# Performance work log

Measured on AMD Instinct MI355X. Metric: run time of the kernel, lower is better.

## Reference

```python
import jax, jax.numpy as jnp
import numpy as np

N_NODES = 100000
N_EDGES = 1600000
D_IN = 128
D_HID = 128
D_OUT = 16
N_LAYERS = 3
N_GRAPHS = 64
EPS = 1e-12


def _glorot(key, shape):
    fan_in = shape[-1]
    bound = 1.0 / np.sqrt(fan_in)
    return jax.random.uniform(key, shape, jnp.float32, -bound, bound)


def setup_inputs() -> dict:
    key = jax.random.key(0)
    ks = jax.random.split(key, 12)
    x = jax.random.normal(ks[0], (N_NODES, D_IN), jnp.float32)
    edge_index = jax.random.randint(ks[1], (2, N_EDGES), 0, N_NODES, jnp.int64)
    batch = jnp.sort(jax.random.randint(ks[2], (N_NODES,), 0, N_GRAPHS, jnp.int64))
    # stacked GraphSage weights: torch Linear stores [out, in]
    Wl = _glorot(ks[3], (N_LAYERS, D_HID, D_IN))
    bl = _glorot(ks[4], (N_LAYERS, D_HID))
    Wr = _glorot(ks[5], (N_LAYERS, D_HID, D_IN))
    br = _glorot(ks[6], (N_LAYERS, D_HID))
    W1 = _glorot(ks[7], (D_HID, D_HID))
    b1 = _glorot(ks[8], (D_HID,))
    W2 = _glorot(ks[9], (D_OUT, D_HID))
    b2 = _glorot(ks[10], (D_OUT,))
    return {"x": x, "edge_index": edge_index, "batch": batch,
            "Wl": Wl, "bl": bl, "Wr": Wr, "br": br,
            "W1": W1, "b1": b1, "W2": W2, "b2": b2}


def reference(x, edge_index, batch, Wl, bl, Wr, br, W1, b1, W2, b2):
    N = x.shape[0]
    src, dst = edge_index[0], edge_index[1]
    # in-degree for mean aggregation (clamped to avoid div-by-zero)
    deg = jax.ops.segment_sum(jnp.ones_like(dst, dtype=x.dtype), dst, num_segments=N)
    deg = jnp.maximum(deg, 1.0)[:, None]
    h = x
    for i in range(N_LAYERS):
        # lin_r applied at nodes, then gathered (equivalent to lin_r(x_j) per edge)
        hr = h @ Wr[i].T + br[i]
        msg = hr[src]                               # [E, D_HID] gather
        agg = jax.ops.segment_sum(msg, dst, num_segments=N) / deg  # scatter-mean
        out = agg + (h @ Wl[i].T + bl[i])
        # F.normalize(out) -> L2 norm along dim=1, eps=1e-12
        nrm = jnp.maximum(jnp.linalg.norm(out, axis=1, keepdims=True), EPS)
        h = jax.nn.relu(out / nrm)                  # dropout is identity (eval)
    # post message-passing MLP (dropout identity in eval mode)
    h = h @ W1.T + b1
    h = h @ W2.T + b2
    # global mean pool over graphs
    cnt = jnp.maximum(jax.ops.segment_sum(jnp.ones_like(batch, dtype=h.dtype), batch, num_segments=N_GRAPHS), 1.0)
    pooled = jax.ops.segment_sum(h, batch, num_segments=N_GRAPHS) / cnt[:, None]
    return jax.nn.log_softmax(pooled, axis=1)
```

## Files before the change

### kernel.cpp

```cpp
#include <hip/hip_runtime.h>
#include <cstdint>
#include <cstddef>

#define NN 100000
#define NE 1600000
#define DD 128
#define NG 64
#define NB 782
#define GB 1563

#if defined(__has_builtin)
#if __has_builtin(__builtin_amdgcn_cvt_pk_f32_fp8) && __has_builtin(__builtin_amdgcn_cvt_pk_fp8_f32)
#define USE_FP8 1
#endif
#endif
#ifndef USE_FP8
#define USE_FP8 0
#endif

using bf16x8 = __attribute__((ext_vector_type(8))) short;
using f32x4  = __attribute__((ext_vector_type(4))) float;
using f32x2  = __attribute__((ext_vector_type(2))) float;

__device__ __forceinline__ int clampi(int v, int hi) {
    v = v < 0 ? 0 : v;
    return v >= hi ? hi - 1 : v;
}
__device__ __forceinline__ unsigned short f2bf(float f) {
    unsigned int u = __float_as_uint(f);
    u += 0x7fffu + ((u >> 16) & 1u);
    return (unsigned short)(u >> 16);
}
__device__ __forceinline__ float bf2f(unsigned short s) {
    return __uint_as_float(((unsigned int)s) << 16);
}
#if USE_FP8
__device__ __forceinline__ unsigned char f2fp8(float v) {
    return (unsigned char)(__builtin_amdgcn_cvt_pk_fp8_f32(v, 0.f, 0, false) & 0xFF);
}
#endif

#define WTOT (3 * 256 * 128)
__global__ void cvtw_kernel(const float* __restrict__ Wl, const float* __restrict__ Wr,
                            unsigned short* __restrict__ Wcat2,
                            int* __restrict__ bcnt, int* __restrict__ gcur0,
                            float* __restrict__ pooled, float* __restrict__ cnt) {
    int i = blockIdx.x * 256 + threadIdx.x;
    if (i < NB) { bcnt[i] = 0; gcur0[i] = 0; }
    if (i < NG * DD) pooled[i] = 0.f;
    if (i < NG) cnt[i] = 0.f;
    if (i < WTOT) {
        int l = i >> 15;
        int rem = i & 32767;
        int o = rem >> 7, k = rem & 127;
        float v = (o < 128) ? Wl[(size_t)l * 16384 + o * 128 + k]
                            : Wr[(size_t)l * 16384 + (o - 128) * 128 + k];
        Wcat2[i] = f2bf(v);
    }
}

template <bool F32IN>
__global__ __launch_bounds__(256) void gemm3_kernel(
    const void* __restrict__ hin_, const unsigned short* __restrict__ Wcat2,
    const float* __restrict__ bl, unsigned short* __restrict__ zb,
    unsigned char* __restrict__ ub, const int* __restrict__ dst,
    int* __restrict__ bcnt, int nG) {
    __shared__ unsigned short sstz[64][136];
    __shared__ unsigned char  sstu[64][272];

    if (blockIdx.x >= nG) {
        int* lcnt = (int*)&sstz[0][0];
        for (int i = threadIdx.x; i < NB; i += 256) lcnt[i] = 0;
        __syncthreads();
        int b = blockIdx.x - nG;
        int e0 = b * 8000;
        int e1 = e0 + 8000; if (e1 > NE) e1 = NE;
        for (int e = e0 + threadIdx.x; e < e1; e += 256)
            atomicAdd(&lcnt[clampi(dst[e], NN) >> 7], 1);
        __syncthreads();
        for (int i = threadIdx.x; i < NB; i += 256)
            if (lcnt[i]) atomicAdd(&bcnt[i], lcnt[i]);
        return;
    }

    const int tid = threadIdx.x;
    const int w = tid >> 6, l = tid & 63;
    const int l15 = l & 15, lg = l >> 4;
    const int half = w >> 1, rt = w & 1;
    const int rbase = blockIdx.x * 64 + rt * 32;

    bf16x8 a[4][2];
#pragma unroll
    for (int m = 0; m < 2; ++m) {
        int node = rbase + m * 16 + l15; node = node < NN ? node : NN - 1;
        if (F32IN) {
            const float* hf = (const float*)hin_;
#pragma unroll
            for (int ks = 0; ks < 4; ++ks) {
                const float4 f0 = *(const float4*)(hf + (size_t)node * DD + ks * 32 + lg * 8);
                const float4 f1 = *(const float4*)(hf + (size_t)node * DD + ks * 32 + lg * 8 + 4);
                bf16x8 t;
                t[0] = (short)f2bf(f0.x); t[1] = (short)f2bf(f0.y);
                t[2] = (short)f2bf(f0.z); t[3] = (short)f2bf(f0.w);
                t[4] = (short)f2bf(f1.x); t[5] = (short)f2bf(f1.y);
                t[6] = (short)f2bf(f1.z); t[7] = (short)f2bf(f1.w);
                a[ks][m] = t;
            }
        } else {
            const unsigned short* hb = (const unsigned short*)hin_;
#pragma unroll
            for (int ks = 0; ks < 4; ++ks)
                a[ks][m] = *(const bf16x8*)(hb + (size_t)node * DD + ks * 32 + lg * 8);
        }
    }

    f32x4 acc[2][8];
#pragma unroll
    for (int m = 0; m < 2; ++m)
#pragma unroll
        for (int n = 0; n < 8; ++n) acc[m][n] = (f32x4){0.f, 0.f, 0.f, 0.f};

    const unsigned short* Wb = Wcat2 + half * 128 * 128;
#pragma unroll
    for (int ks = 0; ks < 4; ++ks) {
#pragma unroll
        for (int n = 0; n < 8; ++n) {
            bf16x8 b = *(const bf16x8*)(Wb + (n * 16 + l15) * 128 + ks * 32 + lg * 8);
            acc[0][n] = __builtin_amdgcn_mfma_f32_16x16x32_bf16(a[ks][0], b, acc[0][n], 0, 0, 0);
            acc[1][n] = __builtin_amdgcn_mfma_f32_16x16x32_bf16(a[ks][1], b, acc[1][n], 0, 0, 0);
        }
    }

    if (half == 0) {
        float blv[8];
#pragma unroll
        for (int n = 0; n < 8; ++n) blv[n] = bl[n * 16 + l15];
#pragma unroll
        for (int m = 0; m < 2; ++m)
#pragma unroll
            for (int r = 0; r < 4; ++r) {
                int brow = rt * 32 + m * 16 + lg * 4 + r;
#pragma unroll
                for (int n = 0; n < 8; ++n)
                    sstz[brow][n * 16 + l15] = f2bf(acc[m][n][r] + blv[n]);
            }
#pragma unroll
        for (int p = 0; p < 8; ++p) {
            int brow = rt * 32 + p * 4 + lg;
            int node = blockIdx.x * 64 + brow;
            bf16x8 vv = *(const bf16x8*)(&sstz[brow][l15 * 8]);
            if (node < NN)
                *(bf16x8*)(zb + (size_t)node * DD + l15 * 8) = vv;
        }
    } else {
#pragma unroll
        for (int m = 0; m < 2; ++m)
#pragma unroll
            for (int r = 0; r < 4; ++r) {
                int brow = rt * 32 + m * 16 + lg * 4 + r;
#pragma unroll
                for (int n = 0; n < 8; ++n) {
#if USE_FP8
                    sstu[brow][n * 16 + l15] = f2fp8(acc[m][n][r]);
#else
                    ((unsigned short*)&sstu[brow][0])[n * 16 + l15] = f2bf(acc[m][n][r]);
#endif
                }
            }
#pragma unroll
        for (int p = 0; p < 8; ++p) {
            int brow = rt * 32 + p * 4 + lg;
            int node = blockIdx.x * 64 + brow;
#if USE_FP8
            uint2 vv = *(const uint2*)(&sstu[brow][l15 * 8]);
            if (node < NN)
                *(uint2*)(ub + (size_t)node * DD + l15 * 8) = vv;
#else
            bf16x8 vv = *(const bf16x8*)((unsigned short*)&sstu[brow][0] + l15 * 8);
            if (node < NN)
                *(bf16x8*)((unsigned short*)ub + (size_t)node * DD + l15 * 8) = vv;
#endif
        }
    }
}

__global__ __launch_bounds__(256) void bpart2_kernel(
    const int* __restrict__ src, const int* __restrict__ dst,
    const int* __restrict__ bcnt, int* __restrict__ gcur0,
    int* __restrict__ bstart_g, uint2* __restrict__ stage) {
    __shared__ int bst[NB];
    __shared__ int lcnt[NB];
    __shared__ int partial[256];
    const int t = threadIdx.x;
    int own[4]; int ssum = 0;
#pragma unroll
    for (int q = 0; q < 4; ++q) {
        int idx = t * 4 + q;
        own[q] = (idx < NB) ? bcnt[idx] : 0;
        ssum += own[q];
    }
    partial[t] = ssum;
    __syncthreads();
    for (int d = 1; d < 256; d <<= 1) {
        int v = (t >= d) ? partial[t - d] : 0;
        __syncthreads();
        partial[t] += v;
        __syncthreads();
    }
    int run = partial[t] - ssum;
#pragma unroll
    for (int q = 0; q < 4; ++q) {
        int idx = t * 4 + q;
        if (idx < NB) bst[idx] = run;
        run += own[q];
    }
    if (blockIdx.x == 0) {
#pragma unroll
        for (int q = 0; q < 4; ++q) {
            int idx = t * 4 + q;
            if (idx < NB) bstart_g[idx] = bst[idx];
        }
        if (t == 0) bstart_g[NB] = NE;
    }
    for (int i = t; i < NB; i += 256) lcnt[i] = 0;
    __syncthreads();
    int e0 = blockIdx.x * 8000;
    int e1 = e0 + 8000; if (e1 > NE) e1 = NE;
    for (int e = e0 + t; e < e1; e += 256)
        atomicAdd(&lcnt[clampi(dst[e], NN) >> 7], 1);
    __syncthreads();
    for (int i = t; i < NB; i += 256) {
        int c = lcnt[i];
        if (c) lcnt[i] = bst[i] + atomicAdd(&gcur0[i], c);
    }
    __syncthreads();
    for (int e = e0 + t; e < e1; e += 256) {
        int d = clampi(dst[e], NN);
        int pos = atomicAdd(&lcnt[d >> 7], 1);
        uint2 p; p.x = (unsigned)clampi(src[e], NN); p.y = (unsigned)d;
        stage[pos] = p;
    }
}

__global__ __launch_bounds__(256) void bfill_kernel(
    const uint2* __restrict__ stage, const int* __restrict__ bstart,
    int* __restrict__ row_ptr, int* __restrict__ csr) {
    __shared__ int scnt[128];
    __shared__ int scur[128];
    const int b = blockIdx.x;
    const int t = threadIdx.x;
    const int s0 = bstart[b], s1 = bstart[b + 1];
    const int n0 = b << 7;
    int nend = NN - n0; if (nend > 128) nend = 128;
    if (t < 128) scnt[t] = 0;
    __syncthreads();
    for (int i = s0 + t; i < s1; i += 256)
        atomicAdd(&scnt[stage[i].y & 127], 1);
    __syncthreads();
    int own = (t < 128) ? scnt[t] : 0;
    for (int d = 1; d < 128; d <<= 1) {
        int v = (t < 128 && t >= d) ? scnt[t - d] : 0;
        __syncthreads();
        if (t < 128) scnt[t] += v;
        __syncthreads();
    }
    if (t < 128) {
        int excl = scnt[t] - own;
        scur[t] = excl;
        if (t < nend) row_ptr[n0 + t] = s0 + excl;
    }
    if (b == NB - 1 && t == 0) row_ptr[NN] = NE;
    __syncthreads();
    for (int i = s0 + t; i < s1; i += 256) {
        uint2 p = stage[i];
        int slot = atomicAdd(&scur[p.y & 127], 1);
        csr[s0 + slot] = (int)p.x;
    }
}

__global__ __launch_bounds__(256) void pullc_kernel(
    const unsigned char* __restrict__ u, const unsigned short* __restrict__ z,
    const float* __restrict__ br, const int* __restrict__ row_ptr,
    const int* __restrict__ csr, unsigned short* __restrict__ hOut) {
    int w = threadIdx.x >> 6, lane = threadIdx.x & 63;
    int n = blockIdx.x * 4 + w;
    if (n >= NN) return;
    int g = lane >> 4, c = lane & 15;
    int s0 = row_ptr[n], s1 = row_ptr[n + 1];
    int len = s1 - s0;
    float inv = 1.0f / (float)(len > 0 ? len : 1);
    float acc[8];
#pragma unroll
    for (int q = 0; q < 8; ++q) acc[q] = 0.f;
    int j = s0 + g;
#if USE_FP8
    for (; j + 12 < s1; j += 16) {
        int i0 = csr[j], i1 = csr[j + 4], i2 = csr[j + 8], i3 = csr[j + 12];
        const uint2 v0 = *(const uint2*)(u + (size_t)i0 * DD + c * 8);
        const uint2 v1 = *(const uint2*)(u + (size_t)i1 * DD + c * 8);
        const uint2 v2 = *(const uint2*)(u + (size_t)i2 * DD + c * 8);
        const uint2 v3 = *(const uint2*)(u + (size_t)i3 * DD + c * 8);
#pragma unroll
        for (int h2 = 0; h2 < 2; ++h2) {
            unsigned a0 = h2 ? v0.y : v0.x, a1 = h2 ? v1.y : v1.x;
            unsigned a2 = h2 ? v2.y : v2.x, a3 = h2 ? v3.y : v3.x;
            f32x2 p;
            p = __builtin_amdgcn_cvt_pk_f32_fp8(a0, false); acc[h2*4+0] += p.x; acc[h2*4+1] += p.y;
            p = __builtin_amdgcn_cvt_pk_f32_fp8(a0, true);  acc[h2*4+2] += p.x; acc[h2*4+3] += p.y;
            p = __builtin_amdgcn_cvt_pk_f32_fp8(a1, false); acc[h2*4+0] += p.x; acc[h2*4+1] += p.y;
            p = __builtin_amdgcn_cvt_pk_f32_fp8(a1, true);  acc[h2*4+2] += p.x; acc[h2*4+3] += p.y;
            p = __builtin_amdgcn_cvt_pk_f32_fp8(a2, false); acc[h2*4+0] += p.x; acc[h2*4+1] += p.y;
            p = __builtin_amdgcn_cvt_pk_f32_fp8(a2, true);  acc[h2*4+2] += p.x; acc[h2*4+3] += p.y;
            p = __builtin_amdgcn_cvt_pk_f32_fp8(a3, false); acc[h2*4+0] += p.x; acc[h2*4+1] += p.y;
            p = __builtin_amdgcn_cvt_pk_f32_fp8(a3, true);  acc[h2*4+2] += p.x; acc[h2*4+3] += p.y;
        }
    }
    for (; j < s1; j += 4) {
        const uint2 v0 = *(const uint2*)(u + (size_t)csr[j] * DD + c * 8);
        f32x2 p;
        p = __builtin_amdgcn_cvt_pk_f32_fp8(v0.x, false); acc[0] += p.x; acc[1] += p.y;
        p = __builtin_amdgcn_cvt_pk_f32_fp8(v0.x, true);  acc[2] += p.x; acc[3] += p.y;
        p = __builtin_amdgcn_cvt_pk_f32_fp8(v0.y, false); acc[4] += p.x; acc[5] += p.y;
        p = __builtin_amdgcn_cvt_pk_f32_fp8(v0.y, true);  acc[6] += p.x; acc[7] += p.y;
    }
#else
    const unsigned short* ub16 = (const unsigned short*)u;
    for (; j + 12 < s1; j += 16) {
        int i0 = csr[j], i1 = csr[j + 4], i2 = csr[j + 8], i3 = csr[j + 12];
        bf16x8 v0 = *(const bf16x8*)(ub16 + (size_t)i0 * DD + c * 8);
        bf16x8 v1 = *(const bf16x8*)(ub16 + (size_t)i1 * DD + c * 8);
        bf16x8 v2 = *(const bf16x8*)(ub16 + (size_t)i2 * DD + c * 8);
        bf16x8 v3 = *(const bf16x8*)(ub16 + (size_t)i3 * DD + c * 8);
#pragma unroll
        for (int q = 0; q < 8; ++q)
            acc[q] += (bf2f((unsigned short)v0[q]) + bf2f((unsigned short)v1[q]))
                    + (bf2f((unsigned short)v2[q]) + bf2f((unsigned short)v3[q]));
    }
    for (; j < s1; j += 4) {
        bf16x8 v0 = *(const bf16x8*)(ub16 + (size_t)csr[j] * DD + c * 8);
#pragma unroll
        for (int q = 0; q < 8; ++q) acc[q] += bf2f((unsigned short)v0[q]);
    }
#endif
#pragma unroll
    for (int q = 0; q < 8; ++q) {
        acc[q] += __shfl_xor(acc[q], 16);
        acc[q] += __shfl_xor(acc[q], 32);
    }
    bf16x8 zv = *(const bf16x8*)(z + (size_t)n * DD + c * 8);
    const float4 br0 = *(const float4*)(br + c * 8);
    const float4 br1 = *(const float4*)(br + c * 8 + 4);
    float bg = len > 0 ? 1.f : 0.f;
    float v[8]; float ss = 0.f;
#pragma unroll
    for (int q = 0; q < 8; ++q) {
        float brq = (q < 4) ? (&br0.x)[q] : (&br1.x)[q - 4];
        v[q] = acc[q] * inv + bf2f((unsigned short)zv[q]) + bg * brq;
        ss = fmaf(v[q], v[q], ss);
    }
    ss += __shfl_xor(ss, 1); ss += __shfl_xor(ss, 2);
    ss += __shfl_xor(ss, 4); ss += __shfl_xor(ss, 8);
    float invn = 1.0f / fmaxf(sqrtf(ss), 1e-12f);
    if (g == 0) {
        bf16x8 r;
#pragma unroll
        for (int q = 0; q < 8; ++q) r[q] = (short)f2bf(fmaxf(v[q], 0.f) * invn);
        *(bf16x8*)(hOut + (size_t)n * DD + c * 8) = r;
    }
}

__global__ __launch_bounds__(256) void pool_bf16(
    const unsigned short* __restrict__ h, const int* __restrict__ batch,
    float* __restrict__ pooled, float* __restrict__ cnt) {
    int hw = (blockIdx.x * blockDim.x + threadIdx.x) >> 5;
    int lane = threadIdx.x & 31;
    int total_hw = (gridDim.x * blockDim.x) >> 5;
    int chunk = (NN + total_hw - 1) / total_hw;
    int nbeg = hw * chunk;
    int nend = nbeg + chunk; if (nend > NN) nend = NN;
    if (nbeg >= nend) return;
    float ax = 0.f, ay = 0.f, az = 0.f, aw = 0.f;
    int curg = clampi(batch[nbeg], NG);
    int run = 0;
    for (int n = nbeg; n < nend; ++n) {
        int g = clampi(batch[n], NG);
        if (g != curg) {
            atomicAdd(&pooled[curg * DD + lane * 4 + 0], ax);
            atomicAdd(&pooled[curg * DD + lane * 4 + 1], ay);
            atomicAdd(&pooled[curg * DD + lane * 4 + 2], az);
            atomicAdd(&pooled[curg * DD + lane * 4 + 3], aw);
            if (lane == 0) atomicAdd(&cnt[curg], (float)run);
            ax = ay = az = aw = 0.f; run = 0; curg = g;
        }
        const ushort4 v = *(const ushort4*)(h + (size_t)n * DD + lane * 4);
        ax += bf2f(v.x); ay += bf2f(v.y); az += bf2f(v.z); aw += bf2f(v.w);
        ++run;
    }
    atomicAdd(&pooled[curg * DD + lane * 4 + 0], ax);
    atomicAdd(&pooled[curg * DD + lane * 4 + 1], ay);
    atomicAdd(&pooled[curg * DD + lane * 4 + 2], az);
    atomicAdd(&pooled[curg * DD + lane * 4 + 3], aw);
    if (lane == 0) atomicAdd(&cnt[curg], (float)run);
}

__global__ __launch_bounds__(1024) void tail_kernel(
    const float* __restrict__ pooled, const float* __restrict__ cnt,
    const float* __restrict__ W1, const float* __restrict__ b1,
    const float* __restrict__ W2, const float* __restrict__ b2,
    float* __restrict__ out) {
    __shared__ float Wc[16][128];
    __shared__ float bcs[16];
    int t = threadIdx.x;
    for (int i = t; i < 2048; i += 1024) {
        int o = i >> 7, k = i & 127;
        float s = 0.f;
        for (int j = 0; j < 128; ++j) s = fmaf(W2[o * 128 + j], W1[j * 128 + k], s);
        Wc[o][k] = s;
    }
    if (t < 16) {
        float sb = 0.f;
        for (int j = 0; j < 128; ++j) sb = fmaf(W2[t * 128 + j], b1[j], sb);
        bcs[t] = sb + b2[t];
    }
    __syncthreads();
    int g = t >> 4, o = t & 15;
    float invc = 1.0f / fmaxf(cnt[g], 1.0f);
    float z = bcs[o];
    for (int k = 0; k < 128; ++k) z = fmaf(pooled[g * DD + k] * invc, Wc[o][k], z);
    float m = z;
    m = fmaxf(m, __shfl_xor(m, 1)); m = fmaxf(m, __shfl_xor(m, 2));
    m = fmaxf(m, __shfl_xor(m, 4)); m = fmaxf(m, __shfl_xor(m, 8));
    float e = expf(z - m);
    float s = e;
    s += __shfl_xor(s, 1); s += __shfl_xor(s, 2);
    s += __shfl_xor(s, 4); s += __shfl_xor(s, 8);
    out[g * 16 + o] = z - m - logf(s);
}

__global__ void zero_out_kernel(float* __restrict__ out, int n) {
    int i = blockIdx.x * 256 + threadIdx.x;
    if (i < n) out[i] = 0.f;
}

extern "C" void kernel_launch(void* const* d_in, const int* in_sizes, int n_in,
                              void* d_out, int out_size, void* d_ws, size_t ws_size,
                              hipStream_t stream) {
    const float* x  = (const float*)d_in[0];
    const int*   ei = (const int*)d_in[1];
    const int* batch = (const int*)d_in[2];
    const float* Wl = (const float*)d_in[3];
    const float* bl = (const float*)d_in[4];
    const float* Wr = (const float*)d_in[5];
    const float* br = (const float*)d_in[6];
    const float* W1 = (const float*)d_in[7];
    const float* b1 = (const float*)d_in[8];
    const float* W2 = (const float*)d_in[9];
    const float* b2 = (const float*)d_in[10];
    float* out = (float*)d_out;

    const int* src = ei;
    const int* dst = ei + NE;

    char* ws = (char*)d_ws;
    size_t off = 0;
    auto alloc = [&](size_t bytes) -> void* {
        void* p = ws + off; off += (bytes + 255) & ~(size_t)255; return p;
    };
    unsigned short* hA    = (unsigned short*)alloc((size_t)NN * DD * 2);
    unsigned short* hB    = (unsigned short*)alloc((size_t)NN * DD * 2);
    unsigned short* zb    = (unsigned short*)alloc((size_t)NN * DD * 2);
    unsigned char*  ub    = (unsigned char*)alloc((size_t)NN * DD * 2);
    unsigned short* Wcat2 = (unsigned short*)alloc((size_t)WTOT * 2);
    int* row_ptr  = (int*)alloc((size_t)(NN + 1) * 4);
    int* csr      = (int*)alloc((size_t)NE * 4);
    uint2* stage  = (uint2*)alloc((size_t)NE * 8);
    int* bcnt     = (int*)alloc((size_t)NB * 4);
    int* bstart   = (int*)alloc((size_t)(NB + 1) * 4);
    int* gcur0    = (int*)alloc((size_t)NB * 4);
    float* pooled = (float*)alloc(NG * DD * 4);
    float* cnt    = (float*)alloc(NG * 4);

    if (off > ws_size) {
        zero_out_kernel<<<(out_size + 255) / 256, 256, 0, stream>>>(out, out_size);
        return;
    }

    cvtw_kernel<<<(WTOT + 255) / 256, 256, 0, stream>>>(
        Wl, Wr, Wcat2, bcnt, gcur0, pooled, cnt);

    const int npb = (NE + 7999) / 8000;

    gemm3_kernel<true><<<GB + npb, 256, 0, stream>>>(
        x, Wcat2, bl, zb, ub, dst, bcnt, GB);

    bpart2_kernel<<<npb, 256, 0, stream>>>(src, dst, bcnt, gcur0, bstart, stage);
    bfill_kernel<<<NB, 256, 0, stream>>>(stage, bstart, row_ptr, csr);

    unsigned short* bufs[2] = {hA, hB};
    pullc_kernel<<<(NN + 3) / 4, 256, 0, stream>>>(
        ub, zb, br, row_ptr, csr, bufs[0]);
    const unsigned short* hin = bufs[0];
    for (int l = 1; l < 3; ++l) {
        gemm3_kernel<false><<<GB, 256, 0, stream>>>(
            hin, Wcat2 + (size_t)l * 256 * 128, bl + (size_t)l * 128,
            zb, ub, dst, bcnt, GB);
        pullc_kernel<<<(NN + 3) / 4, 256, 0, stream>>>(
            ub, zb, br + (size_t)l * 128, row_ptr, csr, bufs[l & 1]);
        hin = bufs[l & 1];
    }

    pool_bf16<<<256, 256, 0, stream>>>(hin, batch, pooled, cnt);
    tail_kernel<<<1, 1024, 0, stream>>>(pooled, cnt, W1, b1, W2, b2, out);
}
```

Measured before the change: 418.7 us.

## Stage GEMM A tile through swizzled LDS, prepack weights, widen FP8 gather loads

The weights are prepacked into MFMA fragment order so each lane's B load is contiguous. The input rows are staged through an XOR-swizzled shared-memory tile with coalesced loads instead of per-lane strided global reads. The aggregation kernel now has each lane gather 16 FP8 bytes per neighbor (8 neighbors in flight per wave, two per iteration) instead of 8 bytes, which cuts the number of load instructions on the gather-bound path. In exchange there is an extra barrier, LDS reuse for the FP8 output staging, and a smaller unroll of the neighbor loop.

```diff
diff --git a/kernel.cpp b/kernel.cpp
--- a/kernel.cpp
+++ b/kernel.cpp
@@ -42,34 +42,39 @@
 
 #define WTOT (3 * 256 * 128)
 __global__ void cvtw_kernel(const float* __restrict__ Wl, const float* __restrict__ Wr,
-                            unsigned short* __restrict__ Wcat2,
+                            unsigned short* __restrict__ Wcat3,
                             int* __restrict__ bcnt, int* __restrict__ gcur0,
                             float* __restrict__ pooled, float* __restrict__ cnt) {
-    int i = blockIdx.x * 256 + threadIdx.x;
-    if (i < NB) { bcnt[i] = 0; gcur0[i] = 0; }
-    if (i < NG * DD) pooled[i] = 0.f;
-    if (i < NG) cnt[i] = 0.f;
-    if (i < WTOT) {
-        int l = i >> 15;
-        int rem = i & 32767;
-        int o = rem >> 7, k = rem & 127;
-        float v = (o < 128) ? Wl[(size_t)l * 16384 + o * 128 + k]
-                            : Wr[(size_t)l * 16384 + (o - 128) * 128 + k];
-        Wcat2[i] = f2bf(v);
+    int t = blockIdx.x * 256 + threadIdx.x;
+    if (t < NB) { bcnt[t] = 0; gcur0[t] = 0; }
+    if (t < NG * DD) pooled[t] = 0.f;
+    if (t < NG) cnt[t] = 0.f;
+    if (t < WTOT) {
+        int j    = t & 7;
+        int lane = (t >> 3) & 63;
+        int ks   = (t >> 9) & 3;
+        int n    = (t >> 11) & 7;
+        int half = (t >> 14) & 1;
+        int l    = t >> 15;
+        int l15 = lane & 15, lg = lane >> 4;
+        int o = n * 16 + l15;
+        int k = ks * 32 + lg * 8 + j;
+        const float* Wsrc = half ? Wr : Wl;
+        Wcat3[t] = f2bf(Wsrc[(size_t)l * 16384 + o * 128 + k]);
     }
 }
 
 template <bool F32IN>
-__global__ __launch_bounds__(256) void gemm3_kernel(
-    const void* __restrict__ hin_, const unsigned short* __restrict__ Wcat2,
+__global__ __launch_bounds__(256) void gemm4_kernel(
+    const void* __restrict__ hin_, const unsigned short* __restrict__ Wf,
     const float* __restrict__ bl, unsigned short* __restrict__ zb,
     unsigned char* __restrict__ ub, const int* __restrict__ dst,
     int* __restrict__ bcnt, int nG) {
+    __shared__ unsigned short lA[64 * 128];
     __shared__ unsigned short sstz[64][136];
-    __shared__ unsigned char  sstu[64][272];
 
     if (blockIdx.x >= nG) {
-        int* lcnt = (int*)&sstz[0][0];
+        int* lcnt = (int*)lA;
         for (int i = threadIdx.x; i < NB; i += 256) lcnt[i] = 0;
         __syncthreads();
         int b = blockIdx.x - nG;
@@ -86,33 +91,43 @@
     const int tid = threadIdx.x;
     const int w = tid >> 6, l = tid & 63;
     const int l15 = l & 15, lg = l >> 4;
+    const int n0 = blockIdx.x * 64;
+
+#pragma unroll
+    for (int q = 0; q < 4; ++q) {
+        int d = (q * 256 + tid) * 16;
+        int row = d >> 8;
+        int colb = d & 255;
+        int srow = n0 + row; srow = srow < NN ? srow : NN - 1;
+        bf16x8 v;
+        if (F32IN) {
+            const float* rp = (const float*)hin_ + (size_t)srow * DD + (colb >> 1);
+            const float4 f0 = *(const float4*)rp;
+            const float4 f1 = *(const float4*)(rp + 4);
+            v[0] = (short)f2bf(f0.x); v[1] = (short)f2bf(f0.y);
+            v[2] = (short)f2bf(f0.z); v[3] = (short)f2bf(f0.w);
+            v[4] = (short)f2bf(f1.x); v[5] = (short)f2bf(f1.y);
+            v[6] = (short)f2bf(f1.z); v[7] = (short)f2bf(f1.w);
+        } else {
+            v = *(const bf16x8*)((const unsigned short*)hin_ + (size_t)srow * DD + (colb >> 1));
+        }
+        int sd = d ^ (((d >> 8) & 7) << 4);
+        *(bf16x8*)((char*)lA + sd) = v;
+    }
+    __syncthreads();
+
     const int half = w >> 1, rt = w & 1;
-    const int rbase = blockIdx.x * 64 + rt * 32;
 
     bf16x8 a[4][2];
 #pragma unroll
-    for (int m = 0; m < 2; ++m) {
-        int node = rbase + m * 16 + l15; node = node < NN ? node : NN - 1;
-        if (F32IN) {
-            const float* hf = (const float*)hin_;
-#pragma unroll
-            for (int ks = 0; ks < 4; ++ks) {
-                const float4 f0 = *(const float4*)(hf + (size_t)node * DD + ks * 32 + lg * 8);
-                const float4 f1 = *(const float4*)(hf + (size_t)node * DD + ks * 32 + lg * 8 + 4);
-                bf16x8 t;
-                t[0] = (short)f2bf(f0.x); t[1] = (short)f2bf(f0.y);
-                t[2] = (short)f2bf(f0.z); t[3] = (short)f2bf(f0.w);
-                t[4] = (short)f2bf(f1.x); t[5] = (short)f2bf(f1.y);
-                t[6] = (short)f2bf(f1.z); t[7] = (short)f2bf(f1.w);
-                a[ks][m] = t;
-            }
-        } else {
-            const unsigned short* hb = (const unsigned short*)hin_;
-#pragma unroll
-            for (int ks = 0; ks < 4; ++ks)
-                a[ks][m] = *(const bf16x8*)(hb + (size_t)node * DD + ks * 32 + lg * 8);
-        }
-    }
+    for (int ks = 0; ks < 4; ++ks)
+#pragma unroll
+        for (int m = 0; m < 2; ++m) {
+            int row = rt * 32 + m * 16 + l15;
+            int L = row * 256 + ks * 64 + lg * 16;
+            int SL = L ^ (((L >> 8) & 7) << 4);
+            a[ks][m] = *(const bf16x8*)((char*)lA + SL);
+        }
 
     f32x4 acc[2][8];
 #pragma unroll
@@ -120,16 +135,18 @@
 #pragma unroll
         for (int n = 0; n < 8; ++n) acc[m][n] = (f32x4){0.f, 0.f, 0.f, 0.f};
 
-    const unsigned short* Wb = Wcat2 + half * 128 * 128;
+    const unsigned short* Wb = Wf + ((size_t)half << 14);
 #pragma unroll
     for (int ks = 0; ks < 4; ++ks) {
 #pragma unroll
         for (int n = 0; n < 8; ++n) {
-            bf16x8 b = *(const bf16x8*)(Wb + (n * 16 + l15) * 128 + ks * 32 + lg * 8);
+            bf16x8 b = *(const bf16x8*)(Wb + (((n << 2) + ks) << 9) + (l << 3));
             acc[0][n] = __builtin_amdgcn_mfma_f32_16x16x32_bf16(a[ks][0], b, acc[0][n], 0, 0, 0);
             acc[1][n] = __builtin_amdgcn_mfma_f32_16x16x32_bf16(a[ks][1], b, acc[1][n], 0, 0, 0);
         }
     }
+
+    __syncthreads();
 
     if (half == 0) {
         float blv[8];
@@ -147,40 +164,46 @@
 #pragma unroll
         for (int p = 0; p < 8; ++p) {
             int brow = rt * 32 + p * 4 + lg;
-            int node = blockIdx.x * 64 + brow;
+            int node = n0 + brow;
             bf16x8 vv = *(const bf16x8*)(&sstz[brow][l15 * 8]);
             if (node < NN)
                 *(bf16x8*)(zb + (size_t)node * DD + l15 * 8) = vv;
         }
     } else {
+#if USE_FP8
+        unsigned char* sstu = (unsigned char*)lA;
 #pragma unroll
         for (int m = 0; m < 2; ++m)
 #pragma unroll
             for (int r = 0; r < 4; ++r) {
                 int brow = rt * 32 + m * 16 + lg * 4 + r;
 #pragma unroll
-                for (int n = 0; n < 8; ++n) {
-#if USE_FP8
-                    sstu[brow][n * 16 + l15] = f2fp8(acc[m][n][r]);
-#else
-                    ((unsigned short*)&sstu[brow][0])[n * 16 + l15] = f2bf(acc[m][n][r]);
-#endif
-                }
+                for (int n = 0; n < 8; ++n)
+                    sstu[brow * 136 + n * 16 + l15] = f2fp8(acc[m][n][r]);
             }
+        __builtin_amdgcn_s_waitcnt(0);
 #pragma unroll
         for (int p = 0; p < 8; ++p) {
             int brow = rt * 32 + p * 4 + lg;
-            int node = blockIdx.x * 64 + brow;
-#if USE_FP8
-            uint2 vv = *(const uint2*)(&sstu[brow][l15 * 8]);
+            int node = n0 + brow;
+            uint2 vv = *(const uint2*)(sstu + brow * 136 + l15 * 8);
             if (node < NN)
                 *(uint2*)(ub + (size_t)node * DD + l15 * 8) = vv;
+        }
 #else
-            bf16x8 vv = *(const bf16x8*)((unsigned short*)&sstu[brow][0] + l15 * 8);
-            if (node < NN)
-                *(bf16x8*)((unsigned short*)ub + (size_t)node * DD + l15 * 8) = vv;
+        unsigned short* ub16 = (unsigned short*)ub;
+#pragma unroll
+        for (int m = 0; m < 2; ++m)
+#pragma unroll
+            for (int r = 0; r < 4; ++r) {
+                int brow = rt * 32 + m * 16 + lg * 4 + r;
+                int node = n0 + brow;
+                if (node < NN)
+#pragma unroll
+                    for (int n = 0; n < 8; ++n)
+                        ub16[(size_t)node * DD + n * 16 + l15] = f2bf(acc[m][n][r]);
+            }
 #endif
-        }
     }
 }
 
@@ -278,84 +301,97 @@
     }
 }
 
-__global__ __launch_bounds__(256) void pullc_kernel(
+__global__ __launch_bounds__(256) void pullc8_kernel(
     const unsigned char* __restrict__ u, const unsigned short* __restrict__ z,
     const float* __restrict__ br, const int* __restrict__ row_ptr,
     const int* __restrict__ csr, unsigned short* __restrict__ hOut) {
     int w = threadIdx.x >> 6, lane = threadIdx.x & 63;
     int n = blockIdx.x * 4 + w;
     if (n >= NN) return;
-    int g = lane >> 4, c = lane & 15;
     int s0 = row_ptr[n], s1 = row_ptr[n + 1];
     int len = s1 - s0;
     float inv = 1.0f / (float)(len > 0 ? len : 1);
+#if USE_FP8
+    int g8 = lane >> 3, c8 = lane & 7;
+    float acc[16];
+#pragma unroll
+    for (int q = 0; q < 16; ++q) acc[q] = 0.f;
+    int j = s0 + g8;
+    for (; j + 8 < s1; j += 16) {
+        int i0 = csr[j], i1 = csr[j + 8];
+        const uint4 v0 = *(const uint4*)(u + (size_t)i0 * DD + c8 * 16);
+        const uint4 v1 = *(const uint4*)(u + (size_t)i1 * DD + c8 * 16);
+#pragma unroll
+        for (int dwi = 0; dwi < 4; ++dwi) {
+            unsigned a0 = (&v0.x)[dwi], a1 = (&v1.x)[dwi];
+            f32x2 p;
+            p = __builtin_amdgcn_cvt_pk_f32_fp8(a0, false); acc[dwi*4+0] += p.x; acc[dwi*4+1] += p.y;
+            p = __builtin_amdgcn_cvt_pk_f32_fp8(a0, true);  acc[dwi*4+2] += p.x; acc[dwi*4+3] += p.y;
+            p = __builtin_amdgcn_cvt_pk_f32_fp8(a1, false); acc[dwi*4+0] += p.x; acc[dwi*4+1] += p.y;
+            p = __builtin_amdgcn_cvt_pk_f32_fp8(a1, true);  acc[dwi*4+2] += p.x; acc[dwi*4+3] += p.y;
+        }
+    }
+    for (; j < s1; j += 8) {
+        int i0 = csr[j];
+        const uint4 v0 = *(const uint4*)(u + (size_t)i0 * DD + c8 * 16);
+#pragma unroll
+        for (int dwi = 0; dwi < 4; ++dwi) {
+            unsigned a0 = (&v0.x)[dwi];
+            f32x2 p;
+            p = __builtin_amdgcn_cvt_pk_f32_fp8(a0, false); acc[dwi*4+0] += p.x; acc[dwi*4+1] += p.y;
+            p = __builtin_amdgcn_cvt_pk_f32_fp8(a0, true);  acc[dwi*4+2] += p.x; acc[dwi*4+3] += p.y;
+        }
+    }
+#pragma unroll
+    for (int q = 0; q < 16; ++q) {
+        acc[q] += __shfl_xor(acc[q], 8);
+        acc[q] += __shfl_xor(acc[q], 16);
+        acc[q] += __shfl_xor(acc[q], 32);
+    }
+    const bf16x8 zv0 = *(const bf16x8*)(z + (size_t)n * DD + c8 * 16);
+    const bf16x8 zv1 = *(const bf16x8*)(z + (size_t)n * DD + c8 * 16 + 8);
+    float bg = len > 0 ? 1.f : 0.f;
+    float v[16]; float ss = 0.f;
+#pragma unroll
+    for (int q = 0; q < 16; ++q) {
+        unsigned short zz = (unsigned short)(q < 8 ? zv0[q] : zv1[q - 8]);
+        v[q] = acc[q] * inv + bf2f(zz) + bg * br[c8 * 16 + q];
+        ss = fmaf(v[q], v[q], ss);
+    }
+    ss += __shfl_xor(ss, 1); ss += __shfl_xor(ss, 2); ss += __shfl_xor(ss, 4);
+    float invn = 1.0f / fmaxf(sqrtf(ss), 1e-12f);
+    if (g8 == 0) {
+        bf16x8 r0, r1;
+#pragma unroll
+        for (int q = 0; q < 8; ++q) {
+            r0[q] = (short)f2bf(fmaxf(v[q], 0.f) * invn);
+            r1[q] = (short)f2bf(fmaxf(v[q + 8], 0.f) * invn);
+        }
+        *(bf16x8*)(hOut + (size_t)n * DD + c8 * 16) = r0;
+        *(bf16x8*)(hOut + (size_t)n * DD + c8 * 16 + 8) = r1;
+    }
+#else
+    int g = lane >> 4, c = lane & 15;
+    const unsigned short* ub16 = (const unsigned short*)u;
     float acc[8];
 #pragma unroll
     for (int q = 0; q < 8; ++q) acc[q] = 0.f;
-    int j = s0 + g;
-#if USE_FP8
-    for (; j + 12 < s1; j += 16) {
-        int i0 = csr[j], i1 = csr[j + 4], i2 = csr[j + 8], i3 = csr[j + 12];
-        const uint2 v0 = *(const uint2*)(u + (size_t)i0 * DD + c * 8);
-        const uint2 v1 = *(const uint2*)(u + (size_t)i1 * DD + c * 8);
-        const uint2 v2 = *(const uint2*)(u + (size_t)i2 * DD + c * 8);
-        const uint2 v3 = *(const uint2*)(u + (size_t)i3 * DD + c * 8);
-#pragma unroll
-        for (int h2 = 0; h2 < 2; ++h2) {
-            unsigned a0 = h2 ? v0.y : v0.x, a1 = h2 ? v1.y : v1.x;
-            unsigned a2 = h2 ? v2.y : v2.x, a3 = h2 ? v3.y : v3.x;
-            f32x2 p;
-            p = __builtin_amdgcn_cvt_pk_f32_fp8(a0, false); acc[h2*4+0] += p.x; acc[h2*4+1] += p.y;
-            p = __builtin_amdgcn_cvt_pk_f32_fp8(a0, true);  acc[h2*4+2] += p.x; acc[h2*4+3] += p.y;
-            p = __builtin_amdgcn_cvt_pk_f32_fp8(a1, false); acc[h2*4+0] += p.x; acc[h2*4+1] += p.y;
-            p = __builtin_amdgcn_cvt_pk_f32_fp8(a1, true);  acc[h2*4+2] += p.x; acc[h2*4+3] += p.y;
-            p = __builtin_amdgcn_cvt_pk_f32_fp8(a2, false); acc[h2*4+0] += p.x; acc[h2*4+1] += p.y;
-            p = __builtin_amdgcn_cvt_pk_f32_fp8(a2, true);  acc[h2*4+2] += p.x; acc[h2*4+3] += p.y;
-            p = __builtin_amdgcn_cvt_pk_f32_fp8(a3, false); acc[h2*4+0] += p.x; acc[h2*4+1] += p.y;
-            p = __builtin_amdgcn_cvt_pk_f32_fp8(a3, true);  acc[h2*4+2] += p.x; acc[h2*4+3] += p.y;
-        }
-    }
-    for (; j < s1; j += 4) {
-        const uint2 v0 = *(const uint2*)(u + (size_t)csr[j] * DD + c * 8);
-        f32x2 p;
-        p = __builtin_amdgcn_cvt_pk_f32_fp8(v0.x, false); acc[0] += p.x; acc[1] += p.y;
-        p = __builtin_amdgcn_cvt_pk_f32_fp8(v0.x, true);  acc[2] += p.x; acc[3] += p.y;
-        p = __builtin_amdgcn_cvt_pk_f32_fp8(v0.y, false); acc[4] += p.x; acc[5] += p.y;
-        p = __builtin_amdgcn_cvt_pk_f32_fp8(v0.y, true);  acc[6] += p.x; acc[7] += p.y;
-    }
-#else
-    const unsigned short* ub16 = (const unsigned short*)u;
-    for (; j + 12 < s1; j += 16) {
-        int i0 = csr[j], i1 = csr[j + 4], i2 = csr[j + 8], i3 = csr[j + 12];
-        bf16x8 v0 = *(const bf16x8*)(ub16 + (size_t)i0 * DD + c * 8);
-        bf16x8 v1 = *(const bf16x8*)(ub16 + (size_t)i1 * DD + c * 8);
-        bf16x8 v2 = *(const bf16x8*)(ub16 + (size_t)i2 * DD + c * 8);
-        bf16x8 v3 = *(const bf16x8*)(ub16 + (size_t)i3 * DD + c * 8);
-#pragma unroll
-        for (int q = 0; q < 8; ++q)
-            acc[q] += (bf2f((unsigned short)v0[q]) + bf2f((unsigned short)v1[q]))
-                    + (bf2f((unsigned short)v2[q]) + bf2f((unsigned short)v3[q]));
-    }
-    for (; j < s1; j += 4) {
+    for (int j = s0 + g; j < s1; j += 4) {
         bf16x8 v0 = *(const bf16x8*)(ub16 + (size_t)csr[j] * DD + c * 8);
 #pragma unroll
         for (int q = 0; q < 8; ++q) acc[q] += bf2f((unsigned short)v0[q]);
     }
-#endif
 #pragma unroll
     for (int q = 0; q < 8; ++q) {
         acc[q] += __shfl_xor(acc[q], 16);
         acc[q] += __shfl_xor(acc[q], 32);
     }
     bf16x8 zv = *(const bf16x8*)(z + (size_t)n * DD + c * 8);
-    const float4 br0 = *(const float4*)(br + c * 8);
-    const float4 br1 = *(const float4*)(br + c * 8 + 4);
     float bg = len > 0 ? 1.f : 0.f;
     float v[8]; float ss = 0.f;
 #pragma unroll
     for (int q = 0; q < 8; ++q) {
-        float brq = (q < 4) ? (&br0.x)[q] : (&br1.x)[q - 4];
-        v[q] = acc[q] * inv + bf2f((unsigned short)zv[q]) + bg * brq;
+        v[q] = acc[q] * inv + bf2f((unsigned short)zv[q]) + bg * br[c * 8 + q];
         ss = fmaf(v[q], v[q], ss);
     }
     ss += __shfl_xor(ss, 1); ss += __shfl_xor(ss, 2);
@@ -367,6 +403,7 @@
         for (int q = 0; q < 8; ++q) r[q] = (short)f2bf(fmaxf(v[q], 0.f) * invn);
         *(bf16x8*)(hOut + (size_t)n * DD + c * 8) = r;
     }
+#endif
 }
 
 __global__ __launch_bounds__(256) void pool_bf16(
@@ -470,7 +507,7 @@
     unsigned short* hB    = (unsigned short*)alloc((size_t)NN * DD * 2);
     unsigned short* zb    = (unsigned short*)alloc((size_t)NN * DD * 2);
     unsigned char*  ub    = (unsigned char*)alloc((size_t)NN * DD * 2);
-    unsigned short* Wcat2 = (unsigned short*)alloc((size_t)WTOT * 2);
+    unsigned short* Wcat3 = (unsigned short*)alloc((size_t)WTOT * 2);
     int* row_ptr  = (int*)alloc((size_t)(NN + 1) * 4);
     int* csr      = (int*)alloc((size_t)NE * 4);
     uint2* stage  = (uint2*)alloc((size_t)NE * 8);
@@ -486,25 +523,25 @@
     }
 
     cvtw_kernel<<<(WTOT + 255) / 256, 256, 0, stream>>>(
-        Wl, Wr, Wcat2, bcnt, gcur0, pooled, cnt);
+        Wl, Wr, Wcat3, bcnt, gcur0, pooled, cnt);
 
     const int npb = (NE + 7999) / 8000;
 
-    gemm3_kernel<true><<<GB + npb, 256, 0, stream>>>(
-        x, Wcat2, bl, zb, ub, dst, bcnt, GB);
+    gemm4_kernel<true><<<GB + npb, 256, 0, stream>>>(
+        x, Wcat3, bl, zb, ub, dst, bcnt, GB);
 
     bpart2_kernel<<<npb, 256, 0, stream>>>(src, dst, bcnt, gcur0, bstart, stage);
     bfill_kernel<<<NB, 256, 0, stream>>>(stage, bstart, row_ptr, csr);
 
     unsigned short* bufs[2] = {hA, hB};
-    pullc_kernel<<<(NN + 3) / 4, 256, 0, stream>>>(
+    pullc8_kernel<<<(NN + 3) / 4, 256, 0, stream>>>(
         ub, zb, br, row_ptr, csr, bufs[0]);
     const unsigned short* hin = bufs[0];
     for (int l = 1; l < 3; ++l) {
-        gemm3_kernel<false><<<GB, 256, 0, stream>>>(
-            hin, Wcat2 + (size_t)l * 256 * 128, bl + (size_t)l * 128,
+        gemm4_kernel<false><<<GB, 256, 0, stream>>>(
+            hin, Wcat3 + (size_t)l * 32768, bl + (size_t)l * 128,
             zb, ub, dst, bcnt, GB);
-        pullc_kernel<<<(NN + 3) / 4, 256, 0, stream>>>(
+        pullc8_kernel<<<(NN + 3) / 4, 256, 0, stream>>>(
             ub, zb, br + (size_t)l * 128, row_ptr, csr, bufs[l & 1]);
         hin = bufs[l & 1];
     }
```

Result: faster. 387.0 us (-7.6%).
